# Kernel tuning notes

Hardware: AMD Instinct MI355X
Metric: run time of the kernel (lower is better)

The kernel has to match this reference:

```python
import jax, jax.numpy as jnp
import numpy as np

S, L, D, H = 4, 2048, 1024, 16
DH = D // H
W_CLUSTER = 384
ROUTING_ITERS = 1
TTOT = S * L


def setup_inputs() -> dict:
    key = jax.random.key(0)
    ks = jax.random.split(key, 8)
    scale = 1.0 / np.sqrt(D)
    return {
        "q_in": jax.random.normal(ks[0], (TTOT, D), jnp.float32),
        "k_in": jax.random.normal(ks[1], (TTOT, D), jnp.float32),
        "v_in": jax.random.normal(ks[2], (TTOT, D), jnp.float32),
        "seqlens_tokens": jnp.full((S,), L, jnp.int32),
        "global_idx_per_set": jax.random.randint(ks[3], (S,), 0, TTOT),
        "Wq": jax.random.normal(ks[4], (D, D), jnp.float32) * scale,
        "Wk": jax.random.normal(ks[5], (D, D), jnp.float32) * scale,
        "Wv": jax.random.normal(ks[6], (D, D), jnp.float32) * scale,
        "Wo": jax.random.normal(ks[7], (D, D), jnp.float32) * scale,
    }


def _l2n(x, eps=1e-6):
    return x / (jnp.linalg.norm(x, axis=-1, keepdims=True) + eps)


def _route_np(r, lens, gidx, w, iters):
    # Host-side per-sequence k-means routing (mirrors the original host-sync loop).
    # Returns augmented token order (global token appended per cluster) and cluster lens.
    bounds = np.concatenate([[0], np.cumsum(lens)])
    order_chunks, len_chunks = [], []
    for s in range(len(lens)):
        a, b = int(bounds[s]), int(bounds[s + 1])
        Ls = b - a
        if Ls <= 0:
            continue
        feats = r[a:b]
        wloc = max(1, min(w, Ls))
        k = max(1, (Ls + wloc - 1) // wloc)
        init_idx = np.clip(np.round(np.linspace(0.0, max(Ls - 1, 0), k)).astype(np.int64), 0, Ls - 1)
        cent = feats[init_idx]
        for _ in range(max(1, iters)):
            sims = feats @ cent.T
            assign = sims.argmax(1)
            sums = np.zeros_like(cent)
            np.add.at(sums, assign, feats)
            counts = np.bincount(assign, minlength=k).astype(cent.dtype)
            cent = sums / np.maximum(counts, 1.0)[:, None]
            cent = cent / (np.linalg.norm(cent, axis=-1, keepdims=True) + 1e-6)
        sims = feats @ cent.T
        assign = sims.argmax(1)
        own = sims[np.arange(Ls), assign]
        order1 = np.argsort(-own, kind="stable")
        assign1 = assign[order1]
        order2 = np.argsort(assign1, kind="stable")
        perm = order1[order2]
        cid = assign1[order2]
        counts = np.bincount(cid, minlength=k)
        keep = np.minimum(counts, wloc)
        starts = np.cumsum(counts) - counts
        pos = np.arange(Ls) - np.repeat(starts, counts)
        keep_mask = pos < keep[cid]
        kept = perm[keep_mask] + a  # absolute kept token indices, cluster-sorted
        kc = keep[keep > 0]
        C = kc.size
        ins = np.cumsum(kc) + np.arange(C)  # insertion slot after each cluster
        total = int(kc.sum()) + C
        wg = np.empty(total, dtype=np.int64)
        m = np.ones(total, dtype=bool)
        m[ins] = False
        wg[m] = kept
        wg[~m] = int(gidx[s])
        order_chunks.append(wg)
        len_chunks.append((kc + 1).astype(np.int64))
    return np.concatenate(order_chunks), np.concatenate(len_chunks)


def _padded_indices(order, lens):
    Ncl, Lmax = lens.size, int(lens.max())
    valid = np.arange(Lmax)[None, :] < lens[:, None]
    idx = np.zeros((Ncl, Lmax), dtype=np.int64)
    idx[valid] = order  # row-major fill matches per-cluster concat order
    return idx, valid


def _attend_and_merge(qh, kh, vh, idx, mask):
    # Padded-varlen non-causal attention per cluster, then mean-merge duplicates.
    scale = 1.0 / np.sqrt(DH)
    qg, kg, vg = qh[idx], kh[idx], vh[idx]  # [Ncl, Lmax, H, Dh]
    scores = jnp.einsum("clhd,cmhd->chlm", qg, kg) * scale
    scores = jnp.where(mask[:, None, None, :], scores, -1e9)
    attn = jax.nn.softmax(scores, axis=-1)
    out = jnp.einsum("chlm,cmhd->clhd", attn, vg)
    out = out * mask[:, :, None, None]
    out_h = jnp.zeros((TTOT, H, DH), out.dtype).at[idx].add(out)
    cnt = jnp.zeros((TTOT,), out.dtype).at[idx].add(mask.astype(out.dtype))
    return out_h / jnp.clip(cnt, 1.0)[:, None, None]


def reference(q_in, k_in, v_in, seqlens_tokens, global_idx_per_set, Wq, Wk, Wv, Wo):
    qh = (q_in @ Wq.T).reshape(TTOT, H, DH)
    kh = (k_in @ Wk.T).reshape(TTOT, H, DH)
    vh = (v_in @ Wv.T).reshape(TTOT, H, DH)
    r = 0.5 * (_l2n(qh.mean(1)) + _l2n(kh.mean(1)))  # routing features (detached in original)
    order, lens = _route_np(np.asarray(r), np.asarray(seqlens_tokens),
                            np.asarray(global_idx_per_set), W_CLUSTER, ROUTING_ITERS)
    idx_np, valid_np = _padded_indices(order, lens)
    idx, mask = jnp.asarray(idx_np), jnp.asarray(valid_np)
    out_h = _attend_and_merge(qh, kh, vh, idx, mask)
    return out_h.reshape(TTOT, D) @ Wo.T
```

## Files before the change

### kernel.cpp

```cpp
#include <hip/hip_runtime.h>
#include <math.h>

#define S_ 4
#define L_ 2048
#define D_ 1024
#define H_ 16
#define DH_ 64
#define TTOT_ 8192
#define WCL_ 384
#define KMAX_ 16
#define MAXCL_ (S_*KMAX_)
#define MAXLEN_ (WCL_+1)
#define LSCAP_ 4096
#define NELEM_ ((size_t)TTOT_*(size_t)D_)

typedef __attribute__((ext_vector_type(8))) short bf16x8;
typedef __attribute__((ext_vector_type(4))) float f32x4;
typedef __attribute__((ext_vector_type(4))) unsigned short u16x4;

__device__ __forceinline__ unsigned short bfh(float x) {
  unsigned u = __float_as_uint(x);
  return (unsigned short)((u + 0x7FFFu + ((u >> 16) & 1u)) >> 16);
}
__device__ __forceinline__ float bff(unsigned short h) {
  return __uint_as_float(((unsigned)h) << 16);
}
__device__ __forceinline__ unsigned pk2(unsigned short a, unsigned short b) {
  return (unsigned)a | ((unsigned)b << 16);
}
#define SWZ(r, c) (((r) << 6) + ((c) ^ (((r) & 7) << 3)))

__device__ __forceinline__ void glds16(const void* g, void* l) {
  __builtin_amdgcn_global_load_lds(
      (const __attribute__((address_space(1))) unsigned int*)g,
      (__attribute__((address_space(3))) unsigned int*)l, 16, 0, 0);
}

__global__ __launch_bounds__(256)
void gemm_feats(const float* __restrict__ Aq, const float* __restrict__ Ak,
                const float* __restrict__ Bq, const float* __restrict__ Bk,
                float* __restrict__ Cq, float* __restrict__ Ck) {
  const float* __restrict__ A = blockIdx.y ? Ak : Aq;
  const float* __restrict__ B = blockIdx.y ? Bk : Bq;
  float* __restrict__ C = blockIdx.y ? Ck : Cq;
  const int Kd = 1024, N = 64;
  __shared__ float As[16][68];
  __shared__ float Bs[16][68];
  const int tx = threadIdx.x & 15, ty = threadIdx.x >> 4;
  const int m0 = blockIdx.x * 64;
  const int lr = threadIdx.x >> 2, lc = threadIdx.x & 3;
  float acc[4][4] = {};
  for (int k0 = 0; k0 < Kd; k0 += 16) {
    __syncthreads();
    float4 a4 = *(const float4*)(A + (size_t)(m0 + lr) * Kd + k0 + lc * 4);
    float4 b4 = *(const float4*)(B + (size_t)lr * Kd + k0 + lc * 4);
    As[lc*4+0][lr] = a4.x; As[lc*4+1][lr] = a4.y; As[lc*4+2][lr] = a4.z; As[lc*4+3][lr] = a4.w;
    Bs[lc*4+0][lr] = b4.x; Bs[lc*4+1][lr] = b4.y; Bs[lc*4+2][lr] = b4.z; Bs[lc*4+3][lr] = b4.w;
    __syncthreads();
#pragma unroll
    for (int kk = 0; kk < 16; kk++) {
      float4 av = *(const float4*)&As[kk][ty * 4];
      float4 bv = *(const float4*)&Bs[kk][tx * 4];
      float aa[4] = {av.x, av.y, av.z, av.w};
      float bb[4] = {bv.x, bv.y, bv.z, bv.w};
#pragma unroll
      for (int i = 0; i < 4; i++)
#pragma unroll
        for (int j = 0; j < 4; j++) acc[i][j] += aa[i] * bb[j];
    }
  }
#pragma unroll
  for (int i = 0; i < 4; i++)
#pragma unroll
    for (int j = 0; j < 4; j++)
      C[(size_t)(m0 + ty * 4 + i) * N + (tx * 4 + j)] = acc[i][j];
}

__device__ __forceinline__
void gemm1_body(const unsigned short* __restrict__ Ah,
                const unsigned short* __restrict__ Bh,
                unsigned short* __restrict__ Ch,
                int b, unsigned char* smem) {
  const int Kd = D_, N = D_;
  const int m0 = (b & 63) * 128, n0 = (b >> 6) * 128;
  unsigned short* LA = (unsigned short*)smem;
  unsigned short* LB = LA + 8192;
  const int tid = threadIdx.x, wave = tid >> 6, lane = tid & 63;
  const int lm = lane & 15, lg = lane >> 4;
  const int wr = wave >> 1, wc = wave & 1;
  const int lrow = lane >> 3;
  const int lchk = (lane & 7) ^ lrow;
  f32x4 acc[4][4];
#pragma unroll
  for (int i = 0; i < 4; i++)
#pragma unroll
    for (int j = 0; j < 4; j++) acc[i][j] = (f32x4){0.f, 0.f, 0.f, 0.f};
  for (int k0 = 0; k0 < Kd; k0 += 64) {
    __syncthreads();
#pragma unroll
    for (int i = 0; i < 4; i++) {
      const int r = wave * 32 + i * 8;
      const size_t ga = (size_t)(m0 + r + lrow) * Kd + k0 + lchk * 8;
      const size_t gb = (size_t)(n0 + r + lrow) * Kd + k0 + lchk * 8;
      glds16(&Ah[ga], &LA[r * 64]);
      glds16(&Bh[gb], &LB[r * 64]);
    }
    __syncthreads();
#pragma unroll
    for (int s = 0; s < 2; s++) {
      bf16x8 ah[4], bh[4];
#pragma unroll
      for (int i = 0; i < 4; i++) {
        const int ra = wr * 64 + i * 16 + lm;
        const int ca = ((s * 4 + lg) ^ (ra & 7)) * 8;
        ah[i] = *(const bf16x8*)&LA[ra * 64 + ca];
        const int rb = wc * 64 + i * 16 + lm;
        const int cb = ((s * 4 + lg) ^ (rb & 7)) * 8;
        bh[i] = *(const bf16x8*)&LB[rb * 64 + cb];
      }
#pragma unroll
      for (int i = 0; i < 4; i++)
#pragma unroll
        for (int j = 0; j < 4; j++)
          acc[i][j] = __builtin_amdgcn_mfma_f32_16x16x32_bf16(ah[i], bh[j], acc[i][j], 0, 0, 0);
    }
  }
#pragma unroll
  for (int i = 0; i < 4; i++)
#pragma unroll
    for (int j = 0; j < 4; j++) {
      const int rowb = m0 + wr * 64 + i * 16 + lg * 4;
      const int col = n0 + wc * 64 + j * 16 + lm;
#pragma unroll
      for (int r = 0; r < 4; r++)
        Ch[(size_t)(rowb + r) * N + col] = bfh(acc[i][j][r]);
    }
}

__global__ __launch_bounds__(256)
void gemm_v(const unsigned short* __restrict__ Ah,
            const unsigned short* __restrict__ Bh, unsigned short* __restrict__ Ch) {
  __shared__ __align__(16) unsigned char smem[49152];
  gemm1_body(Ah, Bh, Ch, blockIdx.x, smem);
}

__global__ __launch_bounds__(256)
void gemm_bf16s2(const unsigned short* __restrict__ Ah, const unsigned short* __restrict__ Al,
                 const unsigned short* __restrict__ Bh,
                 float* __restrict__ C, int M, int N, int Kd) {
  __shared__ __align__(16) unsigned short LA[2][128 * 64];
  __shared__ __align__(16) unsigned short LB[128 * 64];
  const int tid = threadIdx.x, wave = tid >> 6, lane = tid & 63;
  const int lm = lane & 15, lg = lane >> 4;
  const int m0 = blockIdx.x * 128, n0 = blockIdx.y * 128;
  const int wr = wave >> 1, wc = wave & 1;
  const int lrow = lane >> 3;
  const int lchk = (lane & 7) ^ lrow;
  f32x4 acc[4][4];
#pragma unroll
  for (int i = 0; i < 4; i++)
#pragma unroll
    for (int j = 0; j < 4; j++) acc[i][j] = (f32x4){0.f, 0.f, 0.f, 0.f};
  for (int k0 = 0; k0 < Kd; k0 += 64) {
    __syncthreads();
#pragma unroll
    for (int i = 0; i < 4; i++) {
      const int r = wave * 32 + i * 8;
      const size_t ga = (size_t)(m0 + r + lrow) * Kd + k0 + lchk * 8;
      const size_t gb = (size_t)(n0 + r + lrow) * Kd + k0 + lchk * 8;
      glds16(&Ah[ga], &LA[0][r * 64]);
      glds16(&Al[ga], &LA[1][r * 64]);
      glds16(&Bh[gb], &LB[r * 64]);
    }
    __syncthreads();
#pragma unroll
    for (int s = 0; s < 2; s++) {
      bf16x8 ah[4], al[4], bh[4];
#pragma unroll
      for (int i = 0; i < 4; i++) {
        const int ra = wr * 64 + i * 16 + lm;
        const int ca = ((s * 4 + lg) ^ (ra & 7)) * 8;
        ah[i] = *(const bf16x8*)&LA[0][ra * 64 + ca];
        al[i] = *(const bf16x8*)&LA[1][ra * 64 + ca];
        const int rb = wc * 64 + i * 16 + lm;
        const int cb = ((s * 4 + lg) ^ (rb & 7)) * 8;
        bh[i] = *(const bf16x8*)&LB[rb * 64 + cb];
      }
#pragma unroll
      for (int i = 0; i < 4; i++)
#pragma unroll
        for (int j = 0; j < 4; j++) {
          acc[i][j] = __builtin_amdgcn_mfma_f32_16x16x32_bf16(ah[i], bh[j], acc[i][j], 0, 0, 0);
          acc[i][j] = __builtin_amdgcn_mfma_f32_16x16x32_bf16(al[i], bh[j], acc[i][j], 0, 0, 0);
        }
    }
  }
#pragma unroll
  for (int i = 0; i < 4; i++)
#pragma unroll
    for (int j = 0; j < 4; j++) {
      const int rowb = m0 + wr * 64 + i * 16 + lg * 4;
      const int col = n0 + wc * 64 + j * 16 + lm;
#pragma unroll
      for (int r = 0; r < 4; r++)
        C[(size_t)(rowb + r) * N + col] = acc[i][j][r];
    }
}

#define N4W_ ((1 << 20) / 4)
#define N4IN_ ((int)(NELEM_ / 4))
#define NWM_ (64 * 1024)
__global__ __launch_bounds__(256)
void conv_all(const float* __restrict__ Wq, const float* __restrict__ Wk,
              const float* __restrict__ Wv, const float* __restrict__ Wo,
              const float* __restrict__ q_in, const float* __restrict__ k_in,
              const float* __restrict__ v_in,
              unsigned short* __restrict__ WqH, unsigned short* __restrict__ WkH,
              unsigned short* __restrict__ WvH, unsigned short* __restrict__ WoH,
              unsigned short* __restrict__ QSh, unsigned short* __restrict__ KSh,
              unsigned short* __restrict__ VSh,
              float* __restrict__ Wqm, float* __restrict__ Wkm) {
  int i = blockIdx.x * 256 + threadIdx.x;
  if (i < 4 * N4W_) {
    int w = i / N4W_, j = i % N4W_;
    const float* src = (w == 0) ? Wq : (w == 1) ? Wk : (w == 2) ? Wv : Wo;
    unsigned short* dst = (w == 0) ? WqH : (w == 1) ? WkH : (w == 2) ? WvH : WoH;
    float4 v = ((const float4*)src)[j];
    *(uint2*)&dst[(size_t)j * 4] =
        make_uint2(pk2(bfh(v.x), bfh(v.y)), pk2(bfh(v.z), bfh(v.w)));
    return;
  }
  i -= 4 * N4W_;
  if (i < 3 * N4IN_) {
    int w = i / N4IN_, j = i % N4IN_;
    const float* src = (w == 0) ? q_in : (w == 1) ? k_in : v_in;
    unsigned short* dh = (w == 0) ? QSh : (w == 1) ? KSh : VSh;
    float4 v = ((const float4*)src)[j];
    *(uint2*)&dh[(size_t)j * 4] =
        make_uint2(pk2(bfh(v.x), bfh(v.y)), pk2(bfh(v.z), bfh(v.w)));
    return;
  }
  i -= 3 * N4IN_;
  if (i >= 2 * NWM_) return;
  const float* W = (i < NWM_) ? Wq : Wk;
  float* Wm = (i < NWM_) ? Wqm : Wkm;
  int j = i % NWM_;
  int d = j >> 10, kk = j & 1023;
  float s = 0.f;
#pragma unroll
  for (int h = 0; h < 16; h++) s += W[(size_t)(h * 64 + d) * 1024 + kk];
  Wm[j] = s * (1.0f / 16.0f);
}

__global__ __launch_bounds__(256)
void l2comb(const float* __restrict__ FQ, const float* __restrict__ FK,
            float* __restrict__ FE) {
  int t = blockIdx.x * 4 + (threadIdx.x >> 6);
  int lane = threadIdx.x & 63;
  if (t >= TTOT_) return;
  float q = FQ[(size_t)t * 64 + lane], k = FK[(size_t)t * 64 + lane];
  float q2 = q * q, k2 = k * k;
#pragma unroll
  for (int m = 1; m < 64; m <<= 1) {
    q2 += __shfl_xor(q2, m, 64);
    k2 += __shfl_xor(k2, m, 64);
  }
  FE[(size_t)t * 64 + lane] =
      0.5f * (q / (sqrtf(q2) + 1e-6f) + k / (sqrtf(k2) + 1e-6f));
}

__device__ void routing_body(int s, const float* __restrict__ FE,
                             const int* __restrict__ seqlens,
                             const int* __restrict__ gidx, int* __restrict__ cT,
                             int* __restrict__ cL, int* __restrict__ tC,
                             unsigned char* smem) {
  unsigned long long* keys = (unsigned long long*)smem;
  unsigned char* assign = smem + 32768;
  float (*cent)[64] = (float(*)[64])(smem + 36864);
  int* cnt1 = (int*)(smem + 40960);
  int* cnt2 = cnt1 + KMAX_;
  int* starts = cnt2 + KMAX_;

  const int tid = threadIdx.x;
  int a = 0;
  for (int t = 0; t < s; t++) a += seqlens[t];
  int Ls = seqlens[s];
  if (Ls > LSCAP_) Ls = LSCAP_;
  for (int cs = tid; cs < KMAX_; cs += 1024) cL[s * KMAX_ + cs] = 0;
  if (Ls <= 0) return;

  int wloc = Ls < WCL_ ? Ls : WCL_;
  if (wloc < 1) wloc = 1;
  int k = (Ls + wloc - 1) / wloc;
  if (k < 1) k = 1;
  if (k > KMAX_) k = KMAX_;

  if (tid < k * 64) {
    int j = tid >> 6, d = tid & 63;
    double step = (k > 1) ? (double)(Ls - 1) / (double)(k - 1) : 0.0;
    long ii = (long)rint(step * (double)j);
    if (ii < 0) ii = 0;
    if (ii > Ls - 1) ii = Ls - 1;
    cent[j][d] = FE[(size_t)(a + ii) * DH_ + d];
  }
  if (tid < KMAX_) { cnt1[tid] = 0; cnt2[tid] = 0; }
  __syncthreads();

  for (int base2 = 0; base2 < Ls; base2 += 1024) {
    int i = base2 + tid;
    int aj = -1;
    if (i < Ls) {
      const float4* f4 = (const float4*)(FE + (size_t)(a + i) * DH_);
      float4 fr[16];
#pragma unroll
      for (int c4 = 0; c4 < 16; c4++) fr[c4] = f4[c4];
      float best = -1e30f; int bj = 0;
      for (int j = 0; j < k; j++) {
        float sd = 0.f;
#pragma unroll
        for (int c4 = 0; c4 < 16; c4++) {
          float4 cv = *(const float4*)&cent[j][c4 * 4];
          sd += fr[c4].x * cv.x; sd += fr[c4].y * cv.y;
          sd += fr[c4].z * cv.z; sd += fr[c4].w * cv.w;
        }
        if (sd > best) { best = sd; bj = j; }
      }
      assign[i] = (unsigned char)bj;
      aj = bj;
    }
    for (int j = 0; j < k; j++) {
      unsigned long long m = __ballot(aj == j);
      if ((tid & 63) == 0 && m) atomicAdd(&cnt1[j], (int)__popcll(m));
    }
  }
  __syncthreads();

  float csum_acc = 0.f;
  const int jj = tid >> 6, dd = tid & 63;
  if (jj < k) {
    const float* fp = FE + (size_t)a * DH_ + dd;
    int i = 0;
    for (; i + 16 <= Ls; i += 16) {
      float v[16];
#pragma unroll
      for (int u = 0; u < 16; u++) v[u] = fp[(size_t)(i + u) * DH_];
      unsigned char aa[16];
#pragma unroll
      for (int u = 0; u < 16; u++) aa[u] = assign[i + u];
#pragma unroll
      for (int u = 0; u < 16; u++)
        csum_acc += (aa[u] == (unsigned char)jj) ? v[u] : 0.0f;
    }
    for (; i < Ls; i++)
      csum_acc += (assign[i] == (unsigned char)jj) ? fp[(size_t)i * DH_] : 0.0f;
  }
  __syncthreads();
  if (tid < k * 64) {
    float v = csum_acc / fmaxf((float)cnt1[jj], 1.0f);
    float sq = v * v;
#pragma unroll
    for (int m = 1; m < 64; m <<= 1) sq += __shfl_xor(sq, m, 64);
    cent[jj][dd] = v / (sqrtf(sq) + 1e-6f);
  }
  __syncthreads();

  int NP2 = 1;
  while (NP2 < Ls) NP2 <<= 1;
  for (int base2 = 0; base2 < NP2; base2 += 1024) {
    int i = base2 + tid;
    int aj = -1;
    if (i < NP2) {
      unsigned long long key;
      if (i < Ls) {
        const float4* f4 = (const float4*)(FE + (size_t)(a + i) * DH_);
        float4 fr[16];
#pragma unroll
        for (int c4 = 0; c4 < 16; c4++) fr[c4] = f4[c4];
        float best = -1e30f; int bj = 0;
        for (int j = 0; j < k; j++) {
          float sd = 0.f;
#pragma unroll
          for (int c4 = 0; c4 < 16; c4++) {
            float4 cv = *(const float4*)&cent[j][c4 * 4];
            sd += fr[c4].x * cv.x; sd += fr[c4].y * cv.y;
            sd += fr[c4].z * cv.z; sd += fr[c4].w * cv.w;
          }
          if (sd > best) { best = sd; bj = j; }
        }
        aj = bj;
        unsigned int u = __float_as_uint(best);
        unsigned int ord = (u & 0x80000000u) ? ~u : (u | 0x80000000u);
        unsigned int dsc = ~ord;
        key = ((unsigned long long)bj << 45) |
              ((unsigned long long)dsc << 13) | (unsigned long long)i;
      } else {
        key = ~0ull;
      }
      keys[i] = key;
    }
    for (int j = 0; j < k; j++) {
      unsigned long long m = __ballot(aj == j);
      if ((tid & 63) == 0 && m) atomicAdd(&cnt2[j], (int)__popcll(m));
    }
  }
  __syncthreads();

  for (int len2 = 2; len2 <= NP2; len2 <<= 1) {
    for (int st = len2 >> 1; st > 0; st >>= 1) {
      for (int i = tid; i < NP2; i += 1024) {
        int j = i ^ st;
        if (j > i) {
          unsigned long long x = keys[i], y = keys[j];
          bool asc = ((i & len2) == 0);
          if ((x > y) == asc) { keys[i] = y; keys[j] = x; }
        }
      }
      __syncthreads();
    }
  }
  if (tid == 0) {
    starts[0] = 0;
    for (int j = 0; j < k; j++) starts[j + 1] = starts[j] + cnt2[j];
  }
  __syncthreads();

  const int g = gidx[s];
  int cOut = 0;
  for (int j = 0; j < k; j++) {
    int cj = cnt2[j];
    if (cj <= 0) continue;
    int keep = cj < wloc ? cj : wloc;
    int slot = s * KMAX_ + cOut;
    for (int p = tid; p < keep; p += 1024) {
      int token = a + (int)(keys[starts[j] + p] & 0x1FFFull);
      cT[slot * MAXLEN_ + p] = token;
      atomicAdd(&tC[token], 1);
    }
    if (tid == 0) {
      cT[slot * MAXLEN_ + keep] = g;
      atomicAdd(&tC[g], 1);
      cL[slot] = keep + 1;
    }
    cOut++;
  }
}

__global__ __launch_bounds__(1024)
void fused_qkr(const unsigned short* __restrict__ QAh,
               const unsigned short* __restrict__ WqH,
               unsigned short* __restrict__ Qh,
               const unsigned short* __restrict__ KAh,
               const unsigned short* __restrict__ WkH,
               unsigned short* __restrict__ Kh,
               const float* __restrict__ FE, const int* __restrict__ seqlens,
               const int* __restrict__ gidx, int* __restrict__ cT,
               int* __restrict__ cL, int* __restrict__ tC) {
  __shared__ __align__(16) unsigned char smem[49152];
  if (blockIdx.x < 4) {
    routing_body(blockIdx.x, FE, seqlens, gidx, cT, cL, tC, smem);
    return;
  }
  if (threadIdx.x >= 256) return;
  int b = blockIdx.x - 4;
  if (b < 512) {
    gemm1_body(QAh, WqH, Qh, b, smem);
  } else {
    gemm1_body(KAh, WkH, Kh, b - 512, smem);
  }
}

__global__ __launch_bounds__(256)
void attn_kernel(const unsigned short* __restrict__ Qh,
                 const unsigned short* __restrict__ Kh,
                 const unsigned short* __restrict__ Vh,
                 const int* __restrict__ cT, const int* __restrict__ cL,
                 float* __restrict__ OH) {
  const int flat = blockIdx.x;
  const int xcd = flat & 7;
  const int i8 = flat >> 3;
  const int qc = i8 % 7;
  const int g = xcd + 8 * (i8 / 7);
  const int h = g & 15, c = g >> 4;

  const int len = cL[c];
  const int q0 = qc * 64;
  if (len <= 0 || q0 >= len) return;

  __shared__ int toks[MAXLEN_];
  __shared__ __align__(16) unsigned short QP[4096];
  __shared__ __align__(16) unsigned short KT[4096];
  __shared__ __align__(16) unsigned short VT[4096];

  const int tid = threadIdx.x, wave = tid >> 6, lane = tid & 63;
  const int lm = lane & 15, lg = lane >> 4;
  const int lr8 = lane >> 3;
  const int lc8 = (lane & 7) ^ lr8;

  const int krow = tid >> 2;
  const int kc = (tid & 3) * 16;
  const int dg = tid & 15, kg = tid >> 4;
  const int vd0 = dg * 4;

  for (int i = tid; i < len; i += 256) toks[i] = cT[c * MAXLEN_ + i];
  __syncthreads();

  uint4 ka0, ka1;
  u16x4 va0, va1, va2, va3;

#define KV_LOAD(mt_) do {                                                      \
    int kr_ = (mt_) * 64 + krow;                                               \
    int tk_ = toks[kr_ < len ? kr_ : 0];                                       \
    const unsigned short* kph = Kh + (size_t)tk_ * D_ + h * DH_ + kc;          \
    ka0 = *(const uint4*)(kph);  ka1 = *(const uint4*)(kph + 8);               \
    int vr_ = (mt_) * 64 + kg * 4;                                             \
    int t0_ = toks[vr_ + 0 < len ? vr_ + 0 : 0];                               \
    int t1_ = toks[vr_ + 1 < len ? vr_ + 1 : 0];                               \
    int t2_ = toks[vr_ + 2 < len ? vr_ + 2 : 0];                               \
    int t3_ = toks[vr_ + 3 < len ? vr_ + 3 : 0];                               \
    size_t off_ = (size_t)h * DH_ + vd0;                                       \
    va0 = *(const u16x4*)(Vh + (size_t)t0_ * D_ + off_);                       \
    va1 = *(const u16x4*)(Vh + (size_t)t1_ * D_ + off_);                       \
    va2 = *(const u16x4*)(Vh + (size_t)t2_ * D_ + off_);                       \
    va3 = *(const u16x4*)(Vh + (size_t)t3_ * D_ + off_);                       \
  } while (0)

#define KV_WRITE() do {                                                        \
    *(uint4*)&KT[SWZ(krow, kc)] = ka0;                                         \
    *(uint4*)&KT[SWZ(krow, kc + 8)] = ka1;                                     \
    _Pragma("unroll") for (int dd = 0; dd < 4; dd++) {                         \
      *(uint2*)&VT[SWZ(vd0 + dd, kg * 4)] =                                    \
          make_uint2(pk2(va0[dd], va1[dd]), pk2(va2[dd], va3[dd]));            \
    }                                                                          \
  } while (0)

#pragma unroll
  for (int i = 0; i < 2; i++) {
    int slab = wave * 2 + i;
    int r8 = slab * 8;
    int row = q0 + r8 + lr8;
    int tok = toks[row < len ? row : 0];
    glds16(Qh + (size_t)tok * D_ + h * DH_ + lc8 * 8, &QP[r8 * 64]);
  }
  KV_LOAD(0);
  __syncthreads();

  bf16x8 qAh[2];
#pragma unroll
  for (int s = 0; s < 2; s++)
    qAh[s] = *(const bf16x8*)&QP[SWZ(wave * 16 + lm, s * 32 + lg * 8)];

  f32x4 accO[4];
#pragma unroll
  for (int t = 0; t < 4; t++) accO[t] = (f32x4){0.f, 0.f, 0.f, 0.f};
  float mm[4] = {-INFINITY, -INFINITY, -INFINITY, -INFINITY};
  float ll[4] = {0.f, 0.f, 0.f, 0.f};

  const int ntile = (len + 63) >> 6;
  for (int mt = 0; mt < ntile; mt++) {
    __syncthreads();
    KV_WRITE();
    __syncthreads();
    if (mt + 1 < ntile) KV_LOAD(mt + 1);

    f32x4 sA[4];
#pragma unroll
    for (int t = 0; t < 4; t++) sA[t] = (f32x4){0.f, 0.f, 0.f, 0.f};
    __builtin_amdgcn_s_setprio(1);
#pragma unroll
    for (int t = 0; t < 4; t++) {
#pragma unroll
      for (int s = 0; s < 2; s++) {
        bf16x8 kb = *(const bf16x8*)&KT[SWZ(t * 16 + lm, s * 32 + lg * 8)];
        sA[t] = __builtin_amdgcn_mfma_f32_16x16x32_bf16(qAh[s], kb, sA[t], 0, 0, 0);
      }
    }
    __builtin_amdgcn_s_setprio(0);

    float sc[4][4];
#pragma unroll
    for (int t = 0; t < 4; t++) {
      bool kvalid = (mt * 64 + t * 16 + lm) < len;
#pragma unroll
      for (int r = 0; r < 4; r++)
        sc[t][r] = kvalid ? sA[t][r] * 0.125f : -1e9f;
    }
    float mx[4], nn[4], cor[4], sum[4];
#pragma unroll
    for (int r = 0; r < 4; r++) {
      mx[r] = fmaxf(fmaxf(sc[0][r], sc[1][r]), fmaxf(sc[2][r], sc[3][r]));
      mx[r] = fmaxf(mx[r], __shfl_xor(mx[r], 1, 64));
      mx[r] = fmaxf(mx[r], __shfl_xor(mx[r], 2, 64));
      mx[r] = fmaxf(mx[r], __shfl_xor(mx[r], 4, 64));
      mx[r] = fmaxf(mx[r], __shfl_xor(mx[r], 8, 64));
      nn[r] = fmaxf(mm[r], mx[r]);
      cor[r] = __expf(mm[r] - nn[r]);
      mm[r] = nn[r];
    }
    float pp[4][4];
#pragma unroll
    for (int t = 0; t < 4; t++)
#pragma unroll
      for (int r = 0; r < 4; r++) pp[t][r] = __expf(sc[t][r] - nn[r]);
#pragma unroll
    for (int r = 0; r < 4; r++) {
      sum[r] = (pp[0][r] + pp[1][r]) + (pp[2][r] + pp[3][r]);
      sum[r] += __shfl_xor(sum[r], 1, 64);
      sum[r] += __shfl_xor(sum[r], 2, 64);
      sum[r] += __shfl_xor(sum[r], 4, 64);
      sum[r] += __shfl_xor(sum[r], 8, 64);
      ll[r] = ll[r] * cor[r] + sum[r];
    }
#pragma unroll
    for (int t = 0; t < 4; t++) {
#pragma unroll
      for (int r = 0; r < 4; r++) {
        accO[t][r] *= cor[r];
        int row = wave * 16 + lg * 4 + r, col = t * 16 + lm;
        QP[SWZ(row, col)] = bfh(pp[t][r]);
      }
    }

    bf16x8 pAh[2];
#pragma unroll
    for (int s = 0; s < 2; s++)
      pAh[s] = *(const bf16x8*)&QP[SWZ(wave * 16 + lm, s * 32 + lg * 8)];
    __builtin_amdgcn_s_setprio(1);
#pragma unroll
    for (int t = 0; t < 4; t++) {
#pragma unroll
      for (int s = 0; s < 2; s++) {
        bf16x8 vb = *(const bf16x8*)&VT[SWZ(t * 16 + lm, s * 32 + lg * 8)];
        accO[t] = __builtin_amdgcn_mfma_f32_16x16x32_bf16(pAh[s], vb, accO[t], 0, 0, 0);
      }
    }
    __builtin_amdgcn_s_setprio(0);
  }
#undef KV_LOAD
#undef KV_WRITE

#pragma unroll
  for (int t = 0; t < 4; t++) {
#pragma unroll
    for (int r = 0; r < 4; r++) {
      int row = q0 + wave * 16 + lg * 4 + r;
      if (row < len)
        atomicAdd(&OH[(size_t)toks[row] * D_ + h * DH_ + t * 16 + lm],
                  accO[t][r] / ll[r]);
    }
  }
}

__global__ __launch_bounds__(256)
void norm_split(const float* __restrict__ OH, const int* __restrict__ cnt,
                unsigned short* __restrict__ oh, unsigned short* __restrict__ ol) {
  size_t i = (size_t)blockIdx.x * 256 + threadIdx.x;
  size_t n4 = NELEM_ / 4;
  if (i >= n4) return;
  int row = (int)((i * 4) >> 10);
  int cc = cnt[row];
  float s = 1.0f / (float)(cc > 1 ? cc : 1);
  float4 v = ((const float4*)OH)[i];
  v.x *= s; v.y *= s; v.z *= s; v.w *= s;
  unsigned short h0 = bfh(v.x), h1 = bfh(v.y), h2 = bfh(v.z), h3 = bfh(v.w);
  *(uint2*)&oh[i * 4] = make_uint2(pk2(h0, h1), pk2(h2, h3));
  *(uint2*)&ol[i * 4] =
      make_uint2(pk2(bfh(v.x - bff(h0)), bfh(v.y - bff(h1))),
                 pk2(bfh(v.z - bff(h2)), bfh(v.w - bff(h3))));
}

extern "C" void kernel_launch(void* const* d_in, const int* in_sizes, int n_in,
                              void* d_out, int out_size, void* d_ws, size_t ws_size,
                              hipStream_t stream) {
  (void)in_sizes; (void)n_in; (void)out_size; (void)ws_size;
  const float* q_in = (const float*)d_in[0];
  const float* k_in = (const float*)d_in[1];
  const float* v_in = (const float*)d_in[2];
  const int* seqlens = (const int*)d_in[3];
  const int* gidx    = (const int*)d_in[4];
  const float* Wq = (const float*)d_in[5];
  const float* Wk = (const float*)d_in[6];
  const float* Wv = (const float*)d_in[7];
  const float* Wo = (const float*)d_in[8];
  float* out = (float*)d_out;

  unsigned short* Qh = (unsigned short*)d_ws;
  unsigned short* Ql = Qh + NELEM_;
  unsigned short* Kh = Ql + NELEM_;
  unsigned short* Kl = Kh + NELEM_;
  unsigned short* Vh = Kl + NELEM_;
  unsigned short* Vl = Vh + NELEM_;
  float* OH = (float*)(Vl + NELEM_);
  float* WS = OH + NELEM_;
  float* FE = WS + (4 << 19);
  float* FQ = FE + (size_t)TTOT_ * DH_;
  float* FK = FQ + (size_t)TTOT_ * DH_;
  float* Wqm = FK + (size_t)TTOT_ * DH_;
  float* Wkm = Wqm + 64 * 1024;
  int* cT = (int*)(Wkm + 64 * 1024);
  int* cL = cT + MAXCL_ * MAXLEN_;
  int* tC = cL + MAXCL_;

  unsigned short* QSh = (unsigned short*)OH;
  unsigned short* KSh = (unsigned short*)out;
  unsigned short* VSh = Kl;
  unsigned short* WqH = (unsigned short*)WS;
  unsigned short* WkH = WqH + (1 << 20);
  unsigned short* WvH = WkH + (1 << 20);
  unsigned short* WoH = WvH + (1 << 20);
  unsigned short* OHh = Qh;
  unsigned short* OHl = Ql;

  hipMemsetAsync(tC, 0, TTOT_ * sizeof(int), stream);

  dim3 gg(TTOT_ / 128, D_ / 128);

  conv_all<<<(4 * N4W_ + 3 * N4IN_ + 2 * NWM_ + 255) / 256, 256, 0, stream>>>(
      Wq, Wk, Wv, Wo, q_in, k_in, v_in,
      WqH, WkH, WvH, WoH, QSh, KSh, VSh, Wqm, Wkm);

  gemm_feats<<<dim3(TTOT_ / 64, 2), 256, 0, stream>>>(q_in, k_in, Wqm, Wkm, FQ, FK);
  l2comb<<<TTOT_ / 4, 256, 0, stream>>>(FQ, FK, FE);

  fused_qkr<<<4 + 1024, 1024, 0, stream>>>(QSh, WqH, Qh,
                                           KSh, WkH, Kh,
                                           FE, seqlens, gidx, cT, cL, tC);

  gemm_v<<<512, 256, 0, stream>>>(VSh, WvH, Vh);

  hipMemsetAsync(OH, 0, NELEM_ * sizeof(float), stream);
  attn_kernel<<<7 * H_ * MAXCL_, 256, 0, stream>>>(
      Qh, Kh, Vh, cT, cL, OH);

  norm_split<<<(unsigned)((NELEM_ / 4 + 255) / 256), 256, 0, stream>>>(OH, tC, OHh, OHl);
  gemm_bf16s2<<<gg, 256, 0, stream>>>(OHh, OHl, WoH, out, TTOT_, D_, D_);
}
```

Before: 365.6 us.

## Drop split-bf16 output projection and fold V GEMM into fused QK-routing launch

The output projection drops its hi/lo bf16 split of the attention output, so each tile now issues one MFMA per fragment instead of two and loads one A buffer instead of two. The normalization kernel writes only the hi bf16 half. The V projection GEMM moves into the fused Q/K/routing kernel as a third block range, which removes a separate launch and lets V overlap with routing. The cost is lower precision in the final projection, which could push error past tolerance.

After: 335.8 us. 1.09x faster.

```diff
diff --git a/kernel.cpp b/kernel.cpp
--- a/kernel.cpp
+++ b/kernel.cpp
@@ -138,21 +138,15 @@
 }
 
 __global__ __launch_bounds__(256)
-void gemm_v(const unsigned short* __restrict__ Ah,
-            const unsigned short* __restrict__ Bh, unsigned short* __restrict__ Ch) {
-  __shared__ __align__(16) unsigned char smem[49152];
-  gemm1_body(Ah, Bh, Ch, blockIdx.x, smem);
-}
-
-__global__ __launch_bounds__(256)
-void gemm_bf16s2(const unsigned short* __restrict__ Ah, const unsigned short* __restrict__ Al,
-                 const unsigned short* __restrict__ Bh,
-                 float* __restrict__ C, int M, int N, int Kd) {
-  __shared__ __align__(16) unsigned short LA[2][128 * 64];
+void gemm_o1(const unsigned short* __restrict__ Ah,
+             const unsigned short* __restrict__ Bh,
+             float* __restrict__ C) {
+  __shared__ __align__(16) unsigned short LA[128 * 64];
   __shared__ __align__(16) unsigned short LB[128 * 64];
+  const int Kd = D_, N = D_;
   const int tid = threadIdx.x, wave = tid >> 6, lane = tid & 63;
   const int lm = lane & 15, lg = lane >> 4;
-  const int m0 = blockIdx.x * 128, n0 = blockIdx.y * 128;
+  const int m0 = (blockIdx.x & 63) * 128, n0 = (blockIdx.x >> 6) * 128;
   const int wr = wave >> 1, wc = wave & 1;
   const int lrow = lane >> 3;
   const int lchk = (lane & 7) ^ lrow;
@@ -168,20 +162,18 @@
       const int r = wave * 32 + i * 8;
       const size_t ga = (size_t)(m0 + r + lrow) * Kd + k0 + lchk * 8;
       const size_t gb = (size_t)(n0 + r + lrow) * Kd + k0 + lchk * 8;
-      glds16(&Ah[ga], &LA[0][r * 64]);
-      glds16(&Al[ga], &LA[1][r * 64]);
+      glds16(&Ah[ga], &LA[r * 64]);
       glds16(&Bh[gb], &LB[r * 64]);
     }
     __syncthreads();
 #pragma unroll
     for (int s = 0; s < 2; s++) {
-      bf16x8 ah[4], al[4], bh[4];
+      bf16x8 ah[4], bh[4];
 #pragma unroll
       for (int i = 0; i < 4; i++) {
         const int ra = wr * 64 + i * 16 + lm;
         const int ca = ((s * 4 + lg) ^ (ra & 7)) * 8;
-        ah[i] = *(const bf16x8*)&LA[0][ra * 64 + ca];
-        al[i] = *(const bf16x8*)&LA[1][ra * 64 + ca];
+        ah[i] = *(const bf16x8*)&LA[ra * 64 + ca];
         const int rb = wc * 64 + i * 16 + lm;
         const int cb = ((s * 4 + lg) ^ (rb & 7)) * 8;
         bh[i] = *(const bf16x8*)&LB[rb * 64 + cb];
@@ -189,10 +181,8 @@
 #pragma unroll
       for (int i = 0; i < 4; i++)
 #pragma unroll
-        for (int j = 0; j < 4; j++) {
+        for (int j = 0; j < 4; j++)
           acc[i][j] = __builtin_amdgcn_mfma_f32_16x16x32_bf16(ah[i], bh[j], acc[i][j], 0, 0, 0);
-          acc[i][j] = __builtin_amdgcn_mfma_f32_16x16x32_bf16(al[i], bh[j], acc[i][j], 0, 0, 0);
-        }
     }
   }
 #pragma unroll
@@ -446,15 +436,18 @@
 }
 
 __global__ __launch_bounds__(1024)
-void fused_qkr(const unsigned short* __restrict__ QAh,
-               const unsigned short* __restrict__ WqH,
-               unsigned short* __restrict__ Qh,
-               const unsigned short* __restrict__ KAh,
-               const unsigned short* __restrict__ WkH,
-               unsigned short* __restrict__ Kh,
-               const float* __restrict__ FE, const int* __restrict__ seqlens,
-               const int* __restrict__ gidx, int* __restrict__ cT,
-               int* __restrict__ cL, int* __restrict__ tC) {
+void fused_qkvr(const unsigned short* __restrict__ QAh,
+                const unsigned short* __restrict__ WqH,
+                unsigned short* __restrict__ Qh,
+                const unsigned short* __restrict__ KAh,
+                const unsigned short* __restrict__ WkH,
+                unsigned short* __restrict__ Kh,
+                const unsigned short* __restrict__ VAh,
+                const unsigned short* __restrict__ WvH,
+                unsigned short* __restrict__ Vh,
+                const float* __restrict__ FE, const int* __restrict__ seqlens,
+                const int* __restrict__ gidx, int* __restrict__ cT,
+                int* __restrict__ cL, int* __restrict__ tC) {
   __shared__ __align__(16) unsigned char smem[49152];
   if (blockIdx.x < 4) {
     routing_body(blockIdx.x, FE, seqlens, gidx, cT, cL, tC, smem);
@@ -464,8 +457,10 @@
   int b = blockIdx.x - 4;
   if (b < 512) {
     gemm1_body(QAh, WqH, Qh, b, smem);
+  } else if (b < 1024) {
+    gemm1_body(KAh, WkH, Kh, b - 512, smem);
   } else {
-    gemm1_body(KAh, WkH, Kh, b - 512, smem);
+    gemm1_body(VAh, WvH, Vh, b - 1024, smem);
   }
 }
 
@@ -651,8 +646,8 @@
 }
 
 __global__ __launch_bounds__(256)
-void norm_split(const float* __restrict__ OH, const int* __restrict__ cnt,
-                unsigned short* __restrict__ oh, unsigned short* __restrict__ ol) {
+void norm_h(const float* __restrict__ OH, const int* __restrict__ cnt,
+            unsigned short* __restrict__ oh) {
   size_t i = (size_t)blockIdx.x * 256 + threadIdx.x;
   size_t n4 = NELEM_ / 4;
   if (i >= n4) return;
@@ -661,11 +656,8 @@
   float s = 1.0f / (float)(cc > 1 ? cc : 1);
   float4 v = ((const float4*)OH)[i];
   v.x *= s; v.y *= s; v.z *= s; v.w *= s;
-  unsigned short h0 = bfh(v.x), h1 = bfh(v.y), h2 = bfh(v.z), h3 = bfh(v.w);
-  *(uint2*)&oh[i * 4] = make_uint2(pk2(h0, h1), pk2(h2, h3));
-  *(uint2*)&ol[i * 4] =
-      make_uint2(pk2(bfh(v.x - bff(h0)), bfh(v.y - bff(h1))),
-                 pk2(bfh(v.z - bff(h2)), bfh(v.w - bff(h3))));
+  *(uint2*)&oh[i * 4] =
+      make_uint2(pk2(bfh(v.x), bfh(v.y)), pk2(bfh(v.z), bfh(v.w)));
 }
 
 extern "C" void kernel_launch(void* const* d_in, const int* in_sizes, int n_in,
@@ -708,11 +700,8 @@
   unsigned short* WvH = WkH + (1 << 20);
   unsigned short* WoH = WvH + (1 << 20);
   unsigned short* OHh = Qh;
-  unsigned short* OHl = Ql;
 
   hipMemsetAsync(tC, 0, TTOT_ * sizeof(int), stream);
-
-  dim3 gg(TTOT_ / 128, D_ / 128);
 
   conv_all<<<(4 * N4W_ + 3 * N4IN_ + 2 * NWM_ + 255) / 256, 256, 0, stream>>>(
       Wq, Wk, Wv, Wo, q_in, k_in, v_in,
@@ -721,16 +710,15 @@
   gemm_feats<<<dim3(TTOT_ / 64, 2), 256, 0, stream>>>(q_in, k_in, Wqm, Wkm, FQ, FK);
   l2comb<<<TTOT_ / 4, 256, 0, stream>>>(FQ, FK, FE);
 
-  fused_qkr<<<4 + 1024, 1024, 0, stream>>>(QSh, WqH, Qh,
-                                           KSh, WkH, Kh,
-                                           FE, seqlens, gidx, cT, cL, tC);
-
-  gemm_v<<<512, 256, 0, stream>>>(VSh, WvH, Vh);
+  fused_qkvr<<<4 + 1536, 1024, 0, stream>>>(QSh, WqH, Qh,
+                                            KSh, WkH, Kh,
+                                            VSh, WvH, Vh,
+                                            FE, seqlens, gidx, cT, cL, tC);
 
   hipMemsetAsync(OH, 0, NELEM_ * sizeof(float), stream);
   attn_kernel<<<7 * H_ * MAXCL_, 256, 0, stream>>>(
       Qh, Kh, Vh, cT, cL, OH);
 
-  norm_split<<<(unsigned)((NELEM_ / 4 + 255) / 256), 256, 0, stream>>>(OH, tC, OHh, OHl);
-  gemm_bf16s2<<<gg, 256, 0, stream>>>(OHh, OHl, WoH, out, TTOT_, D_, D_);
-}
+  norm_h<<<(unsigned)((NELEM_ / 4 + 255) / 256), 256, 0, stream>>>(OH, tC, OHh);
+  gemm_o1<<<512, 256, 0, stream>>>(OHh, WoH, out);
+}
```
